# Kernel tuning notes

Hardware: AMD Instinct MI355X
Metric: run time of the kernel (lower is better)

The kernel has to match this reference:

```python
import jax, jax.numpy as jnp
import numpy as np

D_MODEL = 256
N_HEADS = 8
HEAD_DIM = D_MODEL // N_HEADS
LN_EPS = 1e-5


def setup_inputs() -> dict:
    key = jax.random.key(0)
    ks = jax.random.split(key, 12)
    B, L = 4, 2048
    s = 1.0 / np.sqrt(D_MODEL)
    inp = {
        "query": jax.random.normal(ks[0], (B, L, D_MODEL), jnp.float32),
        "key": jax.random.normal(ks[1], (B, L, D_MODEL), jnp.float32),
        "value": jax.random.normal(ks[2], (B, L, D_MODEL), jnp.float32),
        "Wq": jax.random.normal(ks[3], (D_MODEL, D_MODEL), jnp.float32) * s,
        "bq": jnp.zeros((D_MODEL,), jnp.float32),
        "Wk": jax.random.normal(ks[4], (D_MODEL, D_MODEL), jnp.float32) * s,
        "bk": jnp.zeros((D_MODEL,), jnp.float32),
        "Wv": jax.random.normal(ks[5], (D_MODEL, D_MODEL), jnp.float32) * s,
        "bv": jnp.zeros((D_MODEL,), jnp.float32),
        "Wo": jax.random.normal(ks[6], (D_MODEL, D_MODEL), jnp.float32) * s,
        "bo": jnp.zeros((D_MODEL,), jnp.float32),
        "ln_g": jnp.ones((D_MODEL,), jnp.float32),
        "ln_b": jnp.zeros((D_MODEL,), jnp.float32),
    }
    return inp


def _split_heads(x):
    B, L, _ = x.shape
    return x.reshape(B, L, N_HEADS, HEAD_DIM).transpose(0, 2, 1, 3)  # [B,H,L,Dh]


def reference(query, key, value, Wq, bq, Wk, bk, Wv, bv, Wo, bo, ln_g, ln_b):
    # torch Linear: x @ W.T + b
    Q = _split_heads(query @ Wq.T + bq)
    K = _split_heads(key @ Wk.T + bk)
    V = _split_heads(value @ Wv.T + bv)
    scores = jnp.einsum("bhqd,bhkd->bhqk", Q, K) / np.sqrt(HEAD_DIM)
    attn = jax.nn.softmax(scores, axis=-1)  # dropout = identity (eval)
    ctx = jnp.einsum("bhqk,bhkd->bhqd", attn, V)
    B, H, L, Dh = ctx.shape
    ctx = ctx.transpose(0, 2, 1, 3).reshape(B, L, D_MODEL)
    out = ctx @ Wo.T + bo
    x = out + query
    mu = jnp.mean(x, axis=-1, keepdims=True)
    var = jnp.mean((x - mu) ** 2, axis=-1, keepdims=True)
    return (x - mu) / jnp.sqrt(var + LN_EPS) * ln_g + ln_b
```

## Files before the change

kernel.cpp:

```cpp
#include <hip/hip_runtime.h>
#include <stdint.h>

#define DM 256
#define NHEADS 8
#define DH 32
#define SEQ 2048
#define NB 4
#define MTOT (NB*SEQ)

#define QSCALE 0.2550351270433207f

typedef __attribute__((ext_vector_type(8))) __bf16 bf16x8;
typedef __attribute__((ext_vector_type(4))) short s16x4;
typedef __attribute__((ext_vector_type(8))) short s16x8;
typedef __attribute__((ext_vector_type(4))) unsigned int u32x4;
typedef __attribute__((ext_vector_type(4))) float f32x4;
typedef __attribute__((ext_vector_type(16))) float f32x16;

__device__ inline short f2bf(float f){
  uint32_t u = __builtin_bit_cast(uint32_t, f);
  u += 0x7fffu + ((u >> 16) & 1u);
  return (short)(u >> 16);
}

__global__ __launch_bounds__(256) void prep(
    const float* __restrict__ Wq, const float* __restrict__ Wk,
    const float* __restrict__ Wv, const float* __restrict__ Wo,
    short* __restrict__ Wqb, short* __restrict__ Wkb,
    short* __restrict__ Wvb, short* __restrict__ Wob)
{
  const int i = (blockIdx.x*256 + threadIdx.x)*8;
  const int seg = i >> 16;
  const int off = i & 65535;
  const float* src = seg==0?Wq: seg==1?Wk: seg==2?Wv:Wo;
  short* dst       = seg==0?Wqb: seg==1?Wkb: seg==2?Wvb:Wob;
  const float sc = (seg==0) ? QSCALE : 1.0f;
  float4 a = *(const float4*)(src + off);
  float4 b = *(const float4*)(src + off + 4);
  s16x8 o;
  o[0]=f2bf(a.x*sc); o[1]=f2bf(a.y*sc); o[2]=f2bf(a.z*sc); o[3]=f2bf(a.w*sc);
  o[4]=f2bf(b.x*sc); o[5]=f2bf(b.y*sc); o[6]=f2bf(b.z*sc); o[7]=f2bf(b.w*sc);
  const int row = off >> 8, col = off & 255;
  const int nf = row >> 4, lrr = row & 15;
  const int kc = col >> 5, lgg = (col >> 3) & 3;
  *(s16x8*)(dst + (((nf*8 + kc)*4 + lgg)*16 + lrr)*8) = o;
}

#define WFRAG(nf_, kc_, lg_, lr_) (((((size_t)(nf_)*8 + (kc_))*4 + (lg_))*16 + (lr_))*8)

__global__ __launch_bounds__(128) void qkv_proj(
    const float* __restrict__ Xq, const float* __restrict__ Xk, const float* __restrict__ Xv,
    const short* __restrict__ Wqb, const short* __restrict__ Wkb, const short* __restrict__ Wvb,
    const float* __restrict__ bq, const float* __restrict__ bk, const float* __restrict__ bv,
    short* __restrict__ Qh, short* __restrict__ Kh, short* __restrict__ Vt)
{
  const int mode = blockIdx.z;
  const float* X    = mode==0 ? Xq : (mode==1 ? Xk : Xv);
  const short* Wb   = mode==0 ? Wqb : (mode==1 ? Wkb : Wvb);
  const float* bias = mode==0 ? bq : (mode==1 ? bk : bv);
  short* dst        = mode==0 ? Qh : (mode==1 ? Kh : Vt);
  const float bscale = (mode==0) ? QSCALE : 1.0f;

  const int wid = threadIdx.x >> 6, lane = threadIdx.x & 63;
  const int lr = lane & 15, lg = lane >> 4;
  const int m0 = blockIdx.x*32 + wid*16;
  const int nf0 = blockIdx.y*8;

  f32x4 acc[8] = {};
  const int bb = m0 >> 11;

  if (mode < 2) {
    #pragma unroll
    for (int kc = 0; kc < 8; ++kc) {
      const int k0 = kc*32 + lg*8;
      const float* ap = X + (size_t)(m0 + lr)*DM + k0;
      float4 a0 = *(const float4*)ap;
      float4 a1 = *(const float4*)(ap + 4);
      bf16x8 a;
      a[0]=(__bf16)a0.x; a[1]=(__bf16)a0.y; a[2]=(__bf16)a0.z; a[3]=(__bf16)a0.w;
      a[4]=(__bf16)a1.x; a[5]=(__bf16)a1.y; a[6]=(__bf16)a1.z; a[7]=(__bf16)a1.w;
      #pragma unroll
      for (int nfi=0; nfi<8; ++nfi) {
        bf16x8 b = *(const bf16x8*)(Wb + WFRAG(nf0+nfi, kc, lg, lr));
        acc[nfi] = __builtin_amdgcn_mfma_f32_16x16x32_bf16(b, a, acc[nfi], 0,0,0);
      }
    }
    const int m = m0 + lr;
    const int l = m & (SEQ-1);
    #pragma unroll
    for (int nfi=0; nfi<8; ++nfi) {
      const int colbase = (nf0+nfi)*16;
      const int h = colbase >> 5;
      const int dbase = (colbase & 31) + lg*4;
      float4 b4 = *(const float4*)(bias + colbase + lg*4);
      s16x4 pk;
      pk[0] = f2bf(acc[nfi][0] + b4.x*bscale);
      pk[1] = f2bf(acc[nfi][1] + b4.y*bscale);
      pk[2] = f2bf(acc[nfi][2] + b4.z*bscale);
      pk[3] = f2bf(acc[nfi][3] + b4.w*bscale);
      *(s16x4*)(dst + ((size_t)(bb*NHEADS + h)*SEQ + l)*DH + dbase) = pk;
    }
  } else {
    #pragma unroll
    for (int kc = 0; kc < 8; ++kc) {
      const int k0 = kc*32 + lg*8;
      const float* ap = X + (size_t)(m0 + lr)*DM + k0;
      float4 a0 = *(const float4*)ap;
      float4 a1 = *(const float4*)(ap + 4);
      bf16x8 a;
      a[0]=(__bf16)a0.x; a[1]=(__bf16)a0.y; a[2]=(__bf16)a0.z; a[3]=(__bf16)a0.w;
      a[4]=(__bf16)a1.x; a[5]=(__bf16)a1.y; a[6]=(__bf16)a1.z; a[7]=(__bf16)a1.w;
      #pragma unroll
      for (int nfi=0; nfi<8; ++nfi) {
        bf16x8 b = *(const bf16x8*)(Wb + WFRAG(nf0+nfi, kc, lg, lr));
        acc[nfi] = __builtin_amdgcn_mfma_f32_16x16x32_bf16(a, b, acc[nfi], 0,0,0);
      }
    }
    const int li0 = (m0 & (SEQ-1)) + lg*4;
    #pragma unroll
    for (int nfi=0; nfi<8; ++nfi) {
      const int col = (nf0+nfi)*16 + lr;
      const float bv_ = bias[col];
      const int h = col >> 5, d = col & 31;
      s16x4 pk;
      #pragma unroll
      for (int r=0;r<4;r++) pk[r] = f2bf(acc[nfi][r] + bv_);
      *(s16x4*)(dst + (((size_t)(bb*NHEADS + h)*(SEQ/32) + (li0>>5))*DH + d)*32 + (li0&31)) = pk;
    }
  }
}

#if __has_builtin(__builtin_amdgcn_permlane32_swap)
typedef unsigned int u32x2v __attribute__((ext_vector_type(2)));
#define PSWAP(a_, b_) do { u32x2v r_ = __builtin_amdgcn_permlane32_swap((a_), (b_), false, false); (a_) = r_[0]; (b_) = r_[1]; } while(0)
#else
#define PSWAP(a_, b_) asm("s_nop 1\n\tv_permlane32_swap_b32 %0, %1" : "+v"(a_), "+v"(b_))
#endif

#define LOADKV(K0_,K1_,V0_,V1_, kvb_) do { \
  const short* kp_ = Kb + (size_t)((kvb_) + l31)*DH + hi8; \
  K0_ = *(const bf16x8*)kp_; K1_ = *(const bf16x8*)(kp_ + 16); \
  const short* vp_ = Vb + ((size_t)(((kvb_) >> 5)*32) + l31)*32 + hi8; \
  V0_ = *(const bf16x8*)vp_; V1_ = *(const bf16x8*)(vp_ + 16); \
} while(0)

#define ATTN_TILE(O_, l_, K0_, K1_, V0_, V1_) do { \
  __builtin_amdgcn_s_setprio(1); \
  f32x16 S_ = __builtin_amdgcn_mfma_f32_32x32x16_bf16(K0_, Q0, zf16, 0,0,0); \
  S_ = __builtin_amdgcn_mfma_f32_32x32x16_bf16(K1_, Q1, S_, 0,0,0); \
  __builtin_amdgcn_s_setprio(0); \
  float p_[16]; \
  _Pragma("unroll") for (int r_=0;r_<16;r_++) p_[r_] = __builtin_amdgcn_exp2f(S_[r_]); \
  l_ += (((p_[0]+p_[1])+(p_[2]+p_[3]))+((p_[4]+p_[5])+(p_[6]+p_[7]))) \
      + (((p_[8]+p_[9])+(p_[10]+p_[11]))+((p_[12]+p_[13])+(p_[14]+p_[15]))); \
  uint32_t pa_, pb_, pc_, pd_; \
  asm("v_cvt_pk_bf16_f32 %0, %1, %2" : "=v"(pa_) : "v"(p_[0]), "v"(p_[1])); \
  asm("v_cvt_pk_bf16_f32 %0, %1, %2" : "=v"(pb_) : "v"(p_[2]), "v"(p_[3])); \
  asm("v_cvt_pk_bf16_f32 %0, %1, %2" : "=v"(pc_) : "v"(p_[4]), "v"(p_[5])); \
  asm("v_cvt_pk_bf16_f32 %0, %1, %2" : "=v"(pd_) : "v"(p_[6]), "v"(p_[7])); \
  PSWAP(pa_, pc_); PSWAP(pb_, pd_); \
  { u32x4 w_ = {pa_, pb_, pc_, pd_}; \
    __builtin_amdgcn_s_setprio(1); \
    O_ = __builtin_amdgcn_mfma_f32_32x32x16_bf16(V0_, __builtin_bit_cast(bf16x8, w_), O_, 0,0,0); \
    __builtin_amdgcn_s_setprio(0); } \
  asm("v_cvt_pk_bf16_f32 %0, %1, %2" : "=v"(pa_) : "v"(p_[8]),  "v"(p_[9])); \
  asm("v_cvt_pk_bf16_f32 %0, %1, %2" : "=v"(pb_) : "v"(p_[10]), "v"(p_[11])); \
  asm("v_cvt_pk_bf16_f32 %0, %1, %2" : "=v"(pc_) : "v"(p_[12]), "v"(p_[13])); \
  asm("v_cvt_pk_bf16_f32 %0, %1, %2" : "=v"(pd_) : "v"(p_[14]), "v"(p_[15])); \
  PSWAP(pa_, pc_); PSWAP(pb_, pd_); \
  { u32x4 w_ = {pa_, pb_, pc_, pd_}; \
    __builtin_amdgcn_s_setprio(1); \
    O_ = __builtin_amdgcn_mfma_f32_32x32x16_bf16(V1_, __builtin_bit_cast(bf16x8, w_), O_, 0,0,0); \
    __builtin_amdgcn_s_setprio(0); } \
} while(0)

__global__ __launch_bounds__(256, 2) void attn(
    const short* __restrict__ Qh, const short* __restrict__ Kh,
    const short* __restrict__ Vt, short* __restrict__ ctx)
{
  const int wid = threadIdx.x >> 6, lane = threadIdx.x & 63;
  const int l31 = lane & 31, hi8 = (lane >> 5)*8;
  const int bh = blockIdx.x;
  const int q0 = blockIdx.y*128 + wid*32;

  const short* Kb = Kh + (size_t)bh*SEQ*DH;
  const short* Vb = Vt + (size_t)bh*SEQ*DH;

  const short* qp = Qh + ((size_t)bh*SEQ + q0 + l31)*DH + hi8;
  const bf16x8 Q0 = *(const bf16x8*)(qp);
  const bf16x8 Q1 = *(const bf16x8*)(qp + 16);

  f32x16 Oa = {}, Ob = {};
  float lrunA = 0.f, lrunB = 0.f;
  const f32x16 zf16 = {};

  bf16x8 Ka0,Ka1,Va0,Va1, Kc0,Kc1,Vc0,Vc1;
  LOADKV(Ka0,Ka1,Va0,Va1, 0);

  #pragma unroll 2
  for (int t = 0; t < 64; t += 2) {
    LOADKV(Kc0,Kc1,Vc0,Vc1, (t+1)*32);
    ATTN_TILE(Oa, lrunA, Ka0,Ka1,Va0,Va1);
    LOADKV(Ka0,Ka1,Va0,Va1, ((t+2)&63)*32);
    ATTN_TILE(Ob, lrunB, Kc0,Kc1,Vc0,Vc1);
  }

  float lrun = lrunA + lrunB;
  lrun += __shfl_xor(lrun, 32);

  const float inv = 1.0f / lrun;
  const int bb = bh >> 3, hh = bh & 7;
  short* cp = ctx + ((size_t)(bb*SEQ) + q0 + l31)*DM + hh*DH + (hi8 >> 1);
  #pragma unroll
  for (int rg=0; rg<4; ++rg) {
    s16x4 o;
    #pragma unroll
    for (int r=0;r<4;r++) o[r] = f2bf((Oa[rg*4+r] + Ob[rg*4+r])*inv);
    *(s16x4*)(cp + rg*8) = o;
  }
}

__global__ __launch_bounds__(256) void out_ln(
    const short* __restrict__ ctx, const short* __restrict__ Wob,
    const float* __restrict__ bo, const float* __restrict__ resid,
    const float* __restrict__ ln_g, const float* __restrict__ ln_b,
    float* __restrict__ out)
{
  __shared__ float2 red[4][16];
  const int wid = threadIdx.x >> 6, lane = threadIdx.x & 63;
  const int lr = lane & 15, lg = lane >> 4;
  const int m0 = blockIdx.x*16;
  const int c0 = wid*64;
  const int m  = m0 + lr;
  const int cb = c0 + lg*4;

  float4 rs_[4], bo_[4], g_[4], b_[4];
  #pragma unroll
  for (int nf=0; nf<4; ++nf) {
    const int col = cb + nf*16;
    bo_[nf] = *(const float4*)(bo + col);
    g_[nf]  = *(const float4*)(ln_g + col);
    b_[nf]  = *(const float4*)(ln_b + col);
    rs_[nf] = *(const float4*)(resid + (size_t)m*DM + col);
  }
  __builtin_amdgcn_sched_barrier(0);

  f32x4 acc[4] = {};
  #pragma unroll
  for (int kc=0; kc<8; ++kc) {
    const int k0 = kc*32 + lg*8;
    bf16x8 a = *(const bf16x8*)(ctx + (size_t)(m0 + lr)*DM + k0);
    #pragma unroll
    for (int nf=0; nf<4; ++nf) {
      bf16x8 b = *(const bf16x8*)(Wob + WFRAG(wid*4+nf, kc, lg, lr));
      acc[nf] = __builtin_amdgcn_mfma_f32_16x16x32_bf16(b, a, acc[nf], 0,0,0);
    }
  }

  float xv[4][4];
  float s = 0.f, s2 = 0.f;
  #pragma unroll
  for (int nf=0; nf<4; ++nf) {
    const float* bp = (const float*)&bo_[nf];
    const float* rp = (const float*)&rs_[nf];
    #pragma unroll
    for (int r=0;r<4;r++) {
      float v = acc[nf][r] + bp[r] + rp[r];
      xv[nf][r] = v; s += v; s2 += v*v;
    }
  }
  s  += __shfl_xor(s, 16);  s  += __shfl_xor(s, 32);
  s2 += __shfl_xor(s2, 16); s2 += __shfl_xor(s2, 32);
  if (lane < 16) red[wid][lr] = make_float2(s, s2);
  __syncthreads();
  s = 0.f; s2 = 0.f;
  #pragma unroll
  for (int w=0;w<4;w++){ float2 t = red[w][lr]; s += t.x; s2 += t.y; }
  const float mean = s * (1.0f/DM);
  const float var  = s2 * (1.0f/DM) - mean*mean;
  const float rstd = rsqrtf(var + 1e-5f);
  #pragma unroll
  for (int nf=0; nf<4; ++nf) {
    const float* gp = (const float*)&g_[nf];
    const float* bp = (const float*)&b_[nf];
    float4 o;
    o.x = (xv[nf][0]-mean)*rstd*gp[0] + bp[0];
    o.y = (xv[nf][1]-mean)*rstd*gp[1] + bp[1];
    o.z = (xv[nf][2]-mean)*rstd*gp[2] + bp[2];
    o.w = (xv[nf][3]-mean)*rstd*gp[3] + bp[3];
    *(float4*)(out + (size_t)m*DM + cb + nf*16) = o;
  }
}

extern "C" void kernel_launch(void* const* d_in, const int* in_sizes, int n_in,
                              void* d_out, int out_size, void* d_ws, size_t ws_size,
                              hipStream_t stream) {
  const float* query = (const float*)d_in[0];
  const float* key   = (const float*)d_in[1];
  const float* value = (const float*)d_in[2];
  const float* Wq    = (const float*)d_in[3];
  const float* bq    = (const float*)d_in[4];
  const float* Wk    = (const float*)d_in[5];
  const float* bk    = (const float*)d_in[6];
  const float* Wv    = (const float*)d_in[7];
  const float* bv    = (const float*)d_in[8];
  const float* Wo    = (const float*)d_in[9];
  const float* bo    = (const float*)d_in[10];
  const float* ln_g  = (const float*)d_in[11];
  const float* ln_b  = (const float*)d_in[12];
  float* out = (float*)d_out;

  const size_t HSZ = (size_t)NB*NHEADS*SEQ*DH;
  short* Qh  = (short*)d_ws;
  short* Kh  = Qh + HSZ;
  short* Vt  = Kh + HSZ;
  short* ctx = Vt + HSZ;
  short* Wqb = ctx + (size_t)MTOT*DM;
  short* Wkb = Wqb + DM*DM;
  short* Wvb = Wkb + DM*DM;
  short* Wob = Wvb + DM*DM;

  prep<<<dim3(128), 256, 0, stream>>>(Wq, Wk, Wv, Wo, Wqb, Wkb, Wvb, Wob);
  qkv_proj<<<dim3(MTOT/32, 2, 3), 128, 0, stream>>>(
      query, key, value, Wqb, Wkb, Wvb, bq, bk, bv, Qh, Kh, Vt);
  attn<<<dim3(NB*NHEADS, SEQ/128), 256, 0, stream>>>(Qh, Kh, Vt, ctx);
  out_ln<<<dim3(MTOT/16), 256, 0, stream>>>(ctx, Wob, bo, query, ln_g, ln_b, out);
}
```

Measured before the change: 66.96 us.

## Pre-pack activations into MFMA fragment layout via separate conversion kernel

Adds an xprep kernel that converts the fp32 query/key/value inputs to bf16 and stores them in the same fragment-tiled layout already used for the weights. qkv_proj then reads one contiguous 16-byte fragment per lane instead of strided fp32 rows with an in-kernel conversion. The attention kernel now writes ctx in the same fragment layout so out_ln can load its A operand contiguously. The cost is an extra kernel launch and an extra full round trip of the three inputs through global memory as bf16. The rounding also changes from plain truncating casts to round-to-nearest-even.

```diff
diff --git a/kernel.cpp b/kernel.cpp
--- a/kernel.cpp
+++ b/kernel.cpp
@@ -22,6 +22,8 @@
   u += 0x7fffu + ((u >> 16) & 1u);
   return (short)(u >> 16);
 }
+
+#define WFRAG(t_, kc_, lg_, lr_) (((((size_t)(t_)*8 + (kc_))*4 + (lg_))*16 + (lr_))*8)
 
 __global__ __launch_bounds__(256) void prep(
     const float* __restrict__ Wq, const float* __restrict__ Wk,
@@ -41,21 +43,35 @@
   o[0]=f2bf(a.x*sc); o[1]=f2bf(a.y*sc); o[2]=f2bf(a.z*sc); o[3]=f2bf(a.w*sc);
   o[4]=f2bf(b.x*sc); o[5]=f2bf(b.y*sc); o[6]=f2bf(b.z*sc); o[7]=f2bf(b.w*sc);
   const int row = off >> 8, col = off & 255;
-  const int nf = row >> 4, lrr = row & 15;
-  const int kc = col >> 5, lgg = (col >> 3) & 3;
-  *(s16x8*)(dst + (((nf*8 + kc)*4 + lgg)*16 + lrr)*8) = o;
-}
-
-#define WFRAG(nf_, kc_, lg_, lr_) (((((size_t)(nf_)*8 + (kc_))*4 + (lg_))*16 + (lr_))*8)
+  *(s16x8*)(dst + WFRAG(row>>4, col>>5, (col>>3)&3, row&15)) = o;
+}
+
+__global__ __launch_bounds__(256) void xprep(
+    const float* __restrict__ Xq, const float* __restrict__ Xk,
+    const float* __restrict__ Xv,
+    short* __restrict__ Xqp, short* __restrict__ Xkp, short* __restrict__ Xvp)
+{
+  const int i = (blockIdx.x*256 + threadIdx.x)*8;
+  const int seg = blockIdx.y;
+  const float* src = seg==0?Xq: seg==1?Xk:Xv;
+  short* dst       = seg==0?Xqp: seg==1?Xkp:Xvp;
+  float4 a = *(const float4*)(src + i);
+  float4 b = *(const float4*)(src + i + 4);
+  s16x8 o;
+  o[0]=f2bf(a.x); o[1]=f2bf(a.y); o[2]=f2bf(a.z); o[3]=f2bf(a.w);
+  o[4]=f2bf(b.x); o[5]=f2bf(b.y); o[6]=f2bf(b.z); o[7]=f2bf(b.w);
+  const int row = i >> 8, col = i & 255;
+  *(s16x8*)(dst + WFRAG(row>>4, col>>5, (col>>3)&3, row&15)) = o;
+}
 
 __global__ __launch_bounds__(128) void qkv_proj(
-    const float* __restrict__ Xq, const float* __restrict__ Xk, const float* __restrict__ Xv,
+    const short* __restrict__ Xqp, const short* __restrict__ Xkp, const short* __restrict__ Xvp,
     const short* __restrict__ Wqb, const short* __restrict__ Wkb, const short* __restrict__ Wvb,
     const float* __restrict__ bq, const float* __restrict__ bk, const float* __restrict__ bv,
     short* __restrict__ Qh, short* __restrict__ Kh, short* __restrict__ Vt)
 {
   const int mode = blockIdx.z;
-  const float* X    = mode==0 ? Xq : (mode==1 ? Xk : Xv);
+  const short* Xp   = mode==0 ? Xqp : (mode==1 ? Xkp : Xvp);
   const short* Wb   = mode==0 ? Wqb : (mode==1 ? Wkb : Wvb);
   const float* bias = mode==0 ? bq : (mode==1 ? bk : bv);
   short* dst        = mode==0 ? Qh : (mode==1 ? Kh : Vt);
@@ -68,17 +84,12 @@
 
   f32x4 acc[8] = {};
   const int bb = m0 >> 11;
+  const int mt = m0 >> 4;
 
   if (mode < 2) {
     #pragma unroll
     for (int kc = 0; kc < 8; ++kc) {
-      const int k0 = kc*32 + lg*8;
-      const float* ap = X + (size_t)(m0 + lr)*DM + k0;
-      float4 a0 = *(const float4*)ap;
-      float4 a1 = *(const float4*)(ap + 4);
-      bf16x8 a;
-      a[0]=(__bf16)a0.x; a[1]=(__bf16)a0.y; a[2]=(__bf16)a0.z; a[3]=(__bf16)a0.w;
-      a[4]=(__bf16)a1.x; a[5]=(__bf16)a1.y; a[6]=(__bf16)a1.z; a[7]=(__bf16)a1.w;
+      bf16x8 a = *(const bf16x8*)(Xp + WFRAG(mt, kc, lg, lr));
       #pragma unroll
       for (int nfi=0; nfi<8; ++nfi) {
         bf16x8 b = *(const bf16x8*)(Wb + WFRAG(nf0+nfi, kc, lg, lr));
@@ -103,13 +114,7 @@
   } else {
     #pragma unroll
     for (int kc = 0; kc < 8; ++kc) {
-      const int k0 = kc*32 + lg*8;
-      const float* ap = X + (size_t)(m0 + lr)*DM + k0;
-      float4 a0 = *(const float4*)ap;
-      float4 a1 = *(const float4*)(ap + 4);
-      bf16x8 a;
-      a[0]=(__bf16)a0.x; a[1]=(__bf16)a0.y; a[2]=(__bf16)a0.z; a[3]=(__bf16)a0.w;
-      a[4]=(__bf16)a1.x; a[5]=(__bf16)a1.y; a[6]=(__bf16)a1.z; a[7]=(__bf16)a1.w;
+      bf16x8 a = *(const bf16x8*)(Xp + WFRAG(mt, kc, lg, lr));
       #pragma unroll
       for (int nfi=0; nfi<8; ++nfi) {
         bf16x8 b = *(const bf16x8*)(Wb + WFRAG(nf0+nfi, kc, lg, lr));
@@ -210,13 +215,16 @@
 
   const float inv = 1.0f / lrun;
   const int bb = bh >> 3, hh = bh & 7;
-  short* cp = ctx + ((size_t)(bb*SEQ) + q0 + l31)*DM + hh*DH + (hi8 >> 1);
+  const int mt8 = (((bb*SEQ) + q0 + l31) >> 4)*8 + hh;
+  const int lrr = l31 & 15;
+  const int j0  = hi8 >> 1;
+  short* cp = ctx + (size_t)mt8*512;
   #pragma unroll
   for (int rg=0; rg<4; ++rg) {
     s16x4 o;
     #pragma unroll
     for (int r=0;r<4;r++) o[r] = f2bf((Oa[rg*4+r] + Ob[rg*4+r])*inv);
-    *(s16x4*)(cp + rg*8) = o;
+    *(s16x4*)(cp + (rg*16 + lrr)*8 + j0) = o;
   }
 }
 
@@ -233,6 +241,7 @@
   const int c0 = wid*64;
   const int m  = m0 + lr;
   const int cb = c0 + lg*4;
+  const int mt = m0 >> 4;
 
   float4 rs_[4], bo_[4], g_[4], b_[4];
   #pragma unroll
@@ -248,8 +257,7 @@
   f32x4 acc[4] = {};
   #pragma unroll
   for (int kc=0; kc<8; ++kc) {
-    const int k0 = kc*32 + lg*8;
-    bf16x8 a = *(const bf16x8*)(ctx + (size_t)(m0 + lr)*DM + k0);
+    bf16x8 a = *(const bf16x8*)(ctx + WFRAG(mt, kc, lg, lr));
     #pragma unroll
     for (int nf=0; nf<4; ++nf) {
       bf16x8 b = *(const bf16x8*)(Wob + WFRAG(wid*4+nf, kc, lg, lr));
@@ -319,10 +327,14 @@
   short* Wkb = Wqb + DM*DM;
   short* Wvb = Wkb + DM*DM;
   short* Wob = Wvb + DM*DM;
+  short* Xqp = Wob + DM*DM;
+  short* Xkp = Xqp + (size_t)MTOT*DM;
+  short* Xvp = Xkp + (size_t)MTOT*DM;
 
   prep<<<dim3(128), 256, 0, stream>>>(Wq, Wk, Wv, Wo, Wqb, Wkb, Wvb, Wob);
+  xprep<<<dim3(1024, 3), 256, 0, stream>>>(query, key, value, Xqp, Xkp, Xvp);
   qkv_proj<<<dim3(MTOT/32, 2, 3), 128, 0, stream>>>(
-      query, key, value, Wqb, Wkb, Wvb, bq, bk, bv, Qh, Kh, Vt);
+      Xqp, Xkp, Xvp, Wqb, Wkb, Wvb, bq, bk, bv, Qh, Kh, Vt);
   attn<<<dim3(NB*NHEADS, SEQ/128), 256, 0, stream>>>(Qh, Kh, Vt, ctx);
   out_ln<<<dim3(MTOT/16), 256, 0, stream>>>(ctx, Wob, bo, query, ln_g, ln_b, out);
 }
```

Measured after the change: 70.04 us. 1.05x slower.
